# Performance work log

Measured on AMD Instinct MI355X. Metric: run time of the kernel, lower is better.

Reference implementation:

```python
import jax, jax.numpy as jnp
import numpy as np

N = 50000      # nodes
E = 800000     # edges (avg degree 16)
F_IN = 128     # num_features
H1 = 256       # hidden_dims[0]
H2 = 128       # hidden_dims[1]
D_EMB = 64     # embedding_dim
C_CLS = 2      # num_classes
EPS = 1e-5     # BatchNorm eps


def setup_inputs() -> dict:
    key = jax.random.key(0)
    ks = jax.random.split(key, 24)
    f32 = jnp.float32
    def w(k, shape, scale=0.05):
        return jax.random.normal(k, shape, f32) * scale
    inp = {
        "x": jax.random.normal(ks[0], (N, F_IN), f32),
        "edge_index": jax.random.randint(ks[1], (2, E), 0, N, jnp.int32),
        # input_proj
        "Wp": w(ks[2], (F_IN, H1)), "bp": jnp.zeros((H1,), f32),
        # conv1 (SAGEConv): lin_l (neighbors, with bias), lin_r (root, no bias)
        "W1l": w(ks[3], (F_IN, H1)), "b1l": jnp.zeros((H1,), f32), "W1r": w(ks[4], (F_IN, H1)),
        # bn1 (eval mode, running stats)
        "bn1_g": jnp.ones((H1,), f32), "bn1_b": jnp.zeros((H1,), f32),
        "bn1_m": w(ks[5], (H1,), 0.01), "bn1_v": jnp.ones((H1,), f32) + 0.1 * jax.random.uniform(ks[6], (H1,), f32),
        # skip_proj
        "Wsk": w(ks[7], (H1, H2)), "bsk": jnp.zeros((H2,), f32),
        # conv2
        "W2l": w(ks[8], (H1, H2)), "b2l": jnp.zeros((H2,), f32), "W2r": w(ks[9], (H1, H2)),
        # bn2
        "bn2_g": jnp.ones((H2,), f32), "bn2_b": jnp.zeros((H2,), f32),
        "bn2_m": w(ks[10], (H2,), 0.01), "bn2_v": jnp.ones((H2,), f32) + 0.1 * jax.random.uniform(ks[11], (H2,), f32),
        # conv3
        "W3l": w(ks[12], (H2, D_EMB)), "b3l": jnp.zeros((D_EMB,), f32), "W3r": w(ks[13], (H2, D_EMB)),
        # classifier
        "Wc": w(ks[14], (D_EMB, C_CLS)), "bc": jnp.zeros((C_CLS,), f32),
    }
    return inp


def _sage(h, src, dst, Wl, bl, Wr):
    # mean aggregation of source features into destination nodes
    s = jax.ops.segment_sum(h[src], dst, num_segments=N)        # [N, d]
    cnt = jax.ops.segment_sum(jnp.ones((src.shape[0], 1), h.dtype), dst, num_segments=N)
    mean = s / jnp.maximum(cnt, 1.0)
    return mean @ Wl + bl + h @ Wr


def _bn(h, g, b, m, v):
    return (h - m) * jax.lax.rsqrt(v + EPS) * g + b


def reference(x, edge_index, Wp, bp, W1l, b1l, W1r, bn1_g, bn1_b, bn1_m, bn1_v,
              Wsk, bsk, W2l, b2l, W2r, bn2_g, bn2_b, bn2_m, bn2_v,
              W3l, b3l, W3r, Wc, bc):
    src, dst = edge_index[0], edge_index[1]
    identity = x @ Wp + bp                                # input_proj
    h = _sage(x, src, dst, W1l, b1l, W1r)                 # conv1
    h = jax.nn.relu(_bn(h, bn1_g, bn1_b, bn1_m, bn1_v) + identity)
    # dropout is identity in eval mode
    identity = h @ Wsk + bsk                              # skip_proj
    h = _sage(h, src, dst, W2l, b2l, W2r)                 # conv2
    h = jax.nn.relu(_bn(h, bn2_g, bn2_b, bn2_m, bn2_v) + identity)
    emb = _sage(h, src, dst, W3l, b3l, W3r)               # conv3
    logits = emb @ Wc + bc
    return (logits, emb)
```

## Files before the change

kernel.cpp:

```cpp
#include <hip/hip_runtime.h>
#include <hip/hip_fp16.h>

#define NN 50000
#define NE 800000
#define SLN 6250
#define CAP 64
#define BCAP 106496
constexpr float EPSV = 1e-5f;

typedef __attribute__((ext_vector_type(8))) short short8;
typedef __attribute__((ext_vector_type(4))) float f32x4;

__device__ __forceinline__ float bf2f(unsigned short u) {
    return __uint_as_float(((unsigned int)u) << 16);
}
__device__ __forceinline__ unsigned short f2bf(float f) {
    unsigned int x = __float_as_uint(f);
    return (unsigned short)((x + 0x7FFFu + ((x >> 16) & 1u)) >> 16);
}
__device__ __forceinline__ unsigned char f2e5(float f) {
    unsigned short h = __half_as_ushort(__float2half(f));
    unsigned short r = h + 0x7F + ((h >> 8) & 1);
    return (unsigned char)(r >> 8);
}
__device__ __forceinline__ void acc16(float* a, uint4 u) {
#pragma unroll
    for (int q = 0; q < 4; q++) {
        unsigned int x = (q == 0) ? u.x : (q == 1) ? u.y : (q == 2) ? u.z : u.w;
        unsigned int h01 = ((x << 8) & 0xFF00u) | ((x << 16) & 0xFF000000u);
        unsigned int h23 = ((x >> 8) & 0xFF00u) | (x & 0xFF000000u);
        __half2 p01 = *(__half2*)&h01, p23 = *(__half2*)&h23;
        float2 f01 = __half22float2(p01), f23 = __half22float2(p23);
        a[q * 4 + 0] += f01.x; a[q * 4 + 1] += f01.y;
        a[q * 4 + 2] += f23.x; a[q * 4 + 3] += f23.y;
    }
}

__global__ __launch_bounds__(256) void k_bin(const int* __restrict__ src,
                                             const int* __restrict__ dst,
                                             int* __restrict__ binCnt,
                                             int2* __restrict__ binBuf) {
    __shared__ int hcnt[8];
    __shared__ int hbase[8];
    int tid = threadIdx.x;
    if (tid < 8) hcnt[tid] = 0;
    __syncthreads();
    int q = blockIdx.x * 256 + tid;
    bool val = q < NE / 4;
    int4 d = make_int4(0, 0, 0, 0), s = make_int4(0, 0, 0, 0);
    int b0 = 0, b1 = 0, b2 = 0, b3 = 0, r0 = 0, r1 = 0, r2 = 0, r3 = 0;
    if (val) {
        d = ((const int4*)dst)[q];
        s = ((const int4*)src)[q];
        b0 = d.x / SLN; r0 = atomicAdd(&hcnt[b0], 1);
        b1 = d.y / SLN; r1 = atomicAdd(&hcnt[b1], 1);
        b2 = d.z / SLN; r2 = atomicAdd(&hcnt[b2], 1);
        b3 = d.w / SLN; r3 = atomicAdd(&hcnt[b3], 1);
    }
    __syncthreads();
    if (tid < 8) hbase[tid] = atomicAdd(&binCnt[tid], hcnt[tid]);
    __syncthreads();
    if (val) {
        binBuf[(size_t)b0 * BCAP + hbase[b0] + r0] = make_int2(d.x, s.x);
        binBuf[(size_t)b1 * BCAP + hbase[b1] + r1] = make_int2(d.y, s.y);
        binBuf[(size_t)b2 * BCAP + hbase[b2] + r2] = make_int2(d.z, s.z);
        binBuf[(size_t)b3 * BCAP + hbase[b3] + r3] = make_int2(d.w, s.w);
    }
}

__global__ __launch_bounds__(256) void k_scatter2(const int2* __restrict__ binBuf,
                                                  const int* __restrict__ binCnt,
                                                  int* __restrict__ cnt,
                                                  int* __restrict__ csr) {
    int bin = blockIdx.x & 7;
    int lb = blockIdx.x >> 3;
    int n = binCnt[bin];
    const int2* buf = binBuf + (size_t)bin * BCAP;
    for (int i = lb * 256 + threadIdx.x; i < n; i += 128 * 256) {
        int2 p = buf[i];
        int slot = atomicAdd(&cnt[p.x], 1);
        csr[p.x * CAP + slot] = p.y;
    }
}

__device__ void prep1_body(int t, const float* Wp, const float* bp, const float* W1l,
                           const float* b1l, const float* W1r, const float* g, const float* b,
                           const float* m, const float* v, unsigned short* Wf, float* c) {
    int lane = t & 63, f = (t >> 6) & 3, kt = (t >> 8) & 7;
    int nb = t >> 11;
    int col = nb * 64 + f * 16 + (lane & 15);
    int k0 = kt * 32 + (lane >> 4) * 8;
    float A = g[col] * rsqrtf(v[col] + EPSV);
    unsigned short* o = Wf + (size_t)t * 8;
    for (int j = 0; j < 8; j++) {
        int k = k0 + j;
        float w;
        if (k < 128) w = W1l[k * 256 + col] * A;
        else         w = W1r[(k - 128) * 256 + col] * A + Wp[(k - 128) * 256 + col];
        o[j] = f2bf(w);
    }
    if (t < 256) {
        float At = g[t] * rsqrtf(v[t] + EPSV);
        c[t] = b1l[t] * At + (b[t] - m[t] * At) + bp[t];
    }
}

__device__ void prep2_body(int t, const float* Wsk, const float* bsk, const float* W2l,
                           const float* b2l, const float* W2r, const float* g, const float* b,
                           const float* m, const float* v, unsigned short* Wf, float* c) {
    int lane = t & 63, f = (t >> 6) & 3, kt = (t >> 8) & 7, nb = t >> 11;
    int col = nb * 64 + f * 16 + (lane & 15);
    int k0 = kt * 32 + (lane >> 4) * 8;
    unsigned short* o = Wf + (size_t)t * 8;
    if (col < 128) {
        float A = g[col] * rsqrtf(v[col] + EPSV);
        for (int j = 0; j < 8; j++) o[j] = f2bf(W2l[(k0 + j) * 128 + col] * A);
    } else {
        int cc = col - 128;
        float A = g[cc] * rsqrtf(v[cc] + EPSV);
        for (int j = 0; j < 8; j++)
            o[j] = f2bf(W2r[(k0 + j) * 128 + cc] * A + Wsk[(k0 + j) * 128 + cc]);
    }
    if (t < 128) {
        float At = g[t] * rsqrtf(v[t] + EPSV);
        c[t] = b2l[t] * At + (b[t] - m[t] * At) + bsk[t];
    }
}

__device__ void prep3_body(int t, const float* W3l, const float* b3l, const float* W3r,
                           unsigned short* Wf, float* c) {
    int lane = t & 63, f = (t >> 6) & 3, kt = (t >> 8) & 3, nb = t >> 10;
    int col = nb * 64 + f * 16 + (lane & 15);
    int k0 = kt * 32 + (lane >> 4) * 8;
    unsigned short* o = Wf + (size_t)t * 8;
    if (col < 64) {
        for (int j = 0; j < 8; j++) o[j] = f2bf(W3l[(k0 + j) * 64 + col]);
    } else {
        int cc = col - 64;
        for (int j = 0; j < 8; j++) o[j] = f2bf(W3r[(k0 + j) * 64 + cc]);
    }
    if (t < 64) c[t] = b3l[t];
}

__global__ void k_prep_fused(const float* x, unsigned short* xcat, unsigned char* xf8,
                             int* cnt, int* binCnt,
                             const float* Wp, const float* bp,
                             const float* W1l, const float* b1l, const float* W1r,
                             const float* g1, const float* b1, const float* m1, const float* v1,
                             const float* Wsk, const float* bsk,
                             const float* W2l, const float* b2l, const float* W2r,
                             const float* g2, const float* b2, const float* m2, const float* v2,
                             const float* W3l, const float* b3l, const float* W3r,
                             unsigned short* Wf1, unsigned short* Wf2, unsigned short* Wf3,
                             float* c1, float* c2, float* c3) {
    int bb = blockIdx.x;
    if (bb < 6250) {
        int i = bb * 256 + threadIdx.x;
        if (i < NN / 4) ((int4*)cnt)[i] = make_int4(0, 0, 0, 0);
        if (i < 2) ((int4*)binCnt)[i] = make_int4(0, 0, 0, 0);
        if (i >= NN * 128 / 4) return;
        int r = i >> 5, c4 = (i & 31) * 4;
        float4 v = ((const float4*)x)[i];
        ushort4 u = make_ushort4(f2bf(v.x), f2bf(v.y), f2bf(v.z), f2bf(v.w));
        *(ushort4*)&xcat[(size_t)r * 256 + 128 + c4] = u;
        uchar4 u8 = make_uchar4(f2e5(v.x), f2e5(v.y), f2e5(v.z), f2e5(v.w));
        *(uchar4*)&xf8[(size_t)r * 128 + c4] = u8;
    } else if (bb < 6282) {
        prep1_body((bb - 6250) * 256 + threadIdx.x, Wp, bp, W1l, b1l, W1r, g1, b1, m1, v1, Wf1, c1);
    } else if (bb < 6314) {
        prep2_body((bb - 6282) * 256 + threadIdx.x, Wsk, bsk, W2l, b2l, W2r, g2, b2, m2, v2, Wf2, c2);
    } else {
        prep3_body((bb - 6314) * 256 + threadIdx.x, W3l, b3l, W3r, Wf3, c3);
    }
}

__global__ __launch_bounds__(256) void k_gemm12(const unsigned short* __restrict__ xcat,
                                                const unsigned short* __restrict__ Wf1,
                                                const float* __restrict__ c1,
                                                const unsigned short* __restrict__ Wf2,
                                                unsigned short* __restrict__ r2,
                                                unsigned char* __restrict__ pf8) {
    constexpr int KT = 8;
    constexpr int HS = 272;
    __shared__ unsigned short Bs[256 * 64];
    __shared__ unsigned short hs[64 * HS];
    int tid = threadIdx.x;
    int lane = tid & 63, w = tid >> 6;
    int bm = blockIdx.x;
    int rbase = bm * 64 + w * 16;

    int ra = rbase + (lane & 15);
    if (ra >= NN) ra = NN - 1;
    const unsigned short* ap = xcat + (size_t)ra * 256 + ((lane >> 4) * 8);
    short8 afr[KT];
#pragma unroll
    for (int kt = 0; kt < KT; kt++) afr[kt] = *(const short8*)(ap + kt * 32);

    int hrow0 = w * 16 + (lane >> 4) * 4;

    for (int nb = 0; nb < 4; nb++) {
        __syncthreads();
        {
            const float4* srcp = (const float4*)(Wf1 + (size_t)nb * 256 * 64);
            float4* dsts = (float4*)Bs;
            for (int i = tid; i < 256 * 8; i += 256) dsts[i] = srcp[i];
        }
        __syncthreads();
        f32x4 acc[4];
#pragma unroll
        for (int f = 0; f < 4; f++) acc[f] = (f32x4){0.f, 0.f, 0.f, 0.f};
#pragma unroll
        for (int kt = 0; kt < KT; kt++) {
#pragma unroll
            for (int f = 0; f < 4; f++) {
                short8 bfr = *(const short8*)&Bs[((kt * 4 + f) * 64 + lane) * 8];
                acc[f] = __builtin_amdgcn_mfma_f32_16x16x32_bf16(afr[kt], bfr, acc[f], 0, 0, 0);
            }
        }
        int cc = nb * 64 + (lane & 15);
#pragma unroll
        for (int f = 0; f < 4; f++) {
            int col = cc + f * 16;
            float bv = c1[col];
#pragma unroll
            for (int r = 0; r < 4; r++) {
                float val = fmaxf(acc[f][r] + bv, 0.f);
                hs[(hrow0 + r) * HS + col] = f2bf(val);
            }
        }
    }

    short8 a2[KT];
    {
        const unsigned short* hp = &hs[(w * 16 + (lane & 15)) * HS + ((lane >> 4) * 8)];
#pragma unroll
        for (int kt = 0; kt < KT; kt++) a2[kt] = *(const short8*)(hp + kt * 32);
    }

    int gr0 = rbase + (lane >> 4) * 4;
    for (int nb = 0; nb < 4; nb++) {
        __syncthreads();
        {
            const float4* srcp = (const float4*)(Wf2 + (size_t)nb * 256 * 64);
            float4* dsts = (float4*)Bs;
            for (int i = tid; i < 256 * 8; i += 256) dsts[i] = srcp[i];
        }
        __syncthreads();
        f32x4 acc[4];
#pragma unroll
        for (int f = 0; f < 4; f++) acc[f] = (f32x4){0.f, 0.f, 0.f, 0.f};
#pragma unroll
        for (int kt = 0; kt < KT; kt++) {
#pragma unroll
            for (int f = 0; f < 4; f++) {
                short8 bfr = *(const short8*)&Bs[((kt * 4 + f) * 64 + lane) * 8];
                acc[f] = __builtin_amdgcn_mfma_f32_16x16x32_bf16(a2[kt], bfr, acc[f], 0, 0, 0);
            }
        }
        int cc = nb * 64 + (lane & 15);
#pragma unroll
        for (int f = 0; f < 4; f++) {
            int col = cc + f * 16;
#pragma unroll
            for (int r = 0; r < 4; r++) {
                int gr = gr0 + r;
                if (gr < NN) {
                    float val = acc[f][r];
                    if (col < 128) pf8[(size_t)gr * 128 + col] = f2e5(val);
                    else           r2[(size_t)gr * 128 + (col - 128)] = f2bf(val);
                }
            }
        }
    }
}

template <int K, int TOTN, int MODE>
__global__ __launch_bounds__(256) void k_gemm(const unsigned short* __restrict__ A,
                                              const unsigned short* __restrict__ Wf,
                                              const float* __restrict__ bias,
                                              unsigned short* __restrict__ Out,
                                              unsigned char* __restrict__ Pf8) {
    constexpr int KT = K / 32;
    constexpr int NB = TOTN / 64;
    __shared__ unsigned short Bs[K * 64];
    int tid = threadIdx.x;
    int lane = tid & 63, w = tid >> 6;
    int bm = blockIdx.x;

    int r0 = bm * 128 + w * 32;
    int ra0 = r0 + (lane & 15);
    int ra1 = ra0 + 16;
    if (ra0 >= NN) ra0 = NN - 1;
    if (ra1 >= NN) ra1 = NN - 1;
    const unsigned short* ap0 = A + (size_t)ra0 * K + ((lane >> 4) * 8);
    const unsigned short* ap1 = A + (size_t)ra1 * K + ((lane >> 4) * 8);
    short8 afr0[KT], afr1[KT];
#pragma unroll
    for (int kt = 0; kt < KT; kt++) {
        afr0[kt] = *(const short8*)(ap0 + kt * 32);
        afr1[kt] = *(const short8*)(ap1 + kt * 32);
    }

    int rb = r0 + (lane >> 4) * 4;

    for (int nb = 0; nb < NB; nb++) {
        __syncthreads();
        {
            const float4* srcp = (const float4*)(Wf + (size_t)nb * K * 64);
            float4* dsts = (float4*)Bs;
            for (int i = tid; i < K * 8; i += 256) dsts[i] = srcp[i];
        }
        __syncthreads();

        f32x4 acc[2][4];
#pragma unroll
        for (int i = 0; i < 2; i++)
#pragma unroll
            for (int f = 0; f < 4; f++) acc[i][f] = (f32x4){0.f, 0.f, 0.f, 0.f};
#pragma unroll
        for (int kt = 0; kt < KT; kt++) {
#pragma unroll
            for (int f = 0; f < 4; f++) {
                short8 bfr = *(const short8*)&Bs[((kt * 4 + f) * 64 + lane) * 8];
                acc[0][f] = __builtin_amdgcn_mfma_f32_16x16x32_bf16(afr0[kt], bfr, acc[0][f], 0, 0, 0);
                acc[1][f] = __builtin_amdgcn_mfma_f32_16x16x32_bf16(afr1[kt], bfr, acc[1][f], 0, 0, 0);
            }
        }

        int cc = nb * 64 + (lane & 15);
#pragma unroll
        for (int af = 0; af < 2; af++) {
#pragma unroll
            for (int f = 0; f < 4; f++) {
#pragma unroll
                for (int r = 0; r < 4; r++) {
                    int gr = rb + af * 16 + r;
                    if (gr < NN) {
                        float val = acc[af][f][r];
                        Out[(size_t)gr * TOTN + cc + f * 16] = f2bf(val);
                    }
                }
            }
        }
    }
}


__global__ __launch_bounds__(256) void k_aggx(const int* __restrict__ cnt,
                                              const int* __restrict__ csr,
                                              const unsigned char* __restrict__ xf8,
                                              unsigned short* __restrict__ xcat) {
    int lane = threadIdx.x & 63, wv = threadIdx.x >> 6;
    int node = blockIdx.x * 4 + wv;
    int deg = cnt[node];
    const int* cp = csr + node * CAP;
    int g = lane >> 3, l8 = lane & 7;
    float a[16];
#pragma unroll
    for (int j = 0; j < 16; j++) a[j] = 0.f;
    const unsigned char* base = xf8 + l8 * 16;
    int e = 0;
    for (; e + 16 <= deg; e += 16) {
        int s0 = cp[e + g], s1 = cp[e + 8 + g];
        uint4 u0 = *(const uint4*)(base + (size_t)s0 * 128);
        uint4 u1 = *(const uint4*)(base + (size_t)s1 * 128);
        acc16(a, u0); acc16(a, u1);
    }
    if (e + g < deg) {
        uint4 u = *(const uint4*)(base + (size_t)cp[e + g] * 128);
        acc16(a, u);
    }
    if (e + 8 + g < deg) {
        uint4 u = *(const uint4*)(base + (size_t)cp[e + 8 + g] * 128);
        acc16(a, u);
    }
#pragma unroll
    for (int j = 0; j < 16; j++) {
        a[j] += __shfl_xor(a[j], 8);
        a[j] += __shfl_xor(a[j], 16);
        a[j] += __shfl_xor(a[j], 32);
    }
    if (lane < 8) {
        float inv = 1.f / (float)max(deg, 1);
        unsigned short o[16];
#pragma unroll
        for (int j = 0; j < 16; j++) o[j] = f2bf(a[j] * inv);
        *(short8*)&xcat[(size_t)node * 256 + lane * 16] = *(short8*)&o[0];
        *(short8*)&xcat[(size_t)node * 256 + lane * 16 + 8] = *(short8*)&o[8];
    }
}

__global__ __launch_bounds__(256) void k_agg2(const unsigned char* __restrict__ pf8,
                                              const unsigned short* __restrict__ r2,
                                              const int* __restrict__ cnt,
                                              const int* __restrict__ csr,
                                              const float* __restrict__ c,
                                              unsigned short* __restrict__ h2) {
    int lane = threadIdx.x & 63, wv = threadIdx.x >> 6;
    int node = blockIdx.x * 4 + wv;
    int deg = cnt[node];
    const int* cp = csr + node * CAP;
    int g = lane >> 3, l8 = lane & 7;
    float a[16];
#pragma unroll
    for (int j = 0; j < 16; j++) a[j] = 0.f;
    const unsigned char* base = pf8 + l8 * 16;
    int e = 0;
    for (; e + 16 <= deg; e += 16) {
        int s0 = cp[e + g], s1 = cp[e + 8 + g];
        uint4 u0 = *(const uint4*)(base + (size_t)s0 * 128);
        uint4 u1 = *(const uint4*)(base + (size_t)s1 * 128);
        acc16(a, u0); acc16(a, u1);
    }
    if (e + g < deg) {
        uint4 u = *(const uint4*)(base + (size_t)cp[e + g] * 128);
        acc16(a, u);
    }
    if (e + 8 + g < deg) {
        uint4 u = *(const uint4*)(base + (size_t)cp[e + 8 + g] * 128);
        acc16(a, u);
    }
#pragma unroll
    for (int j = 0; j < 16; j++) {
        a[j] += __shfl_xor(a[j], 8);
        a[j] += __shfl_xor(a[j], 16);
        a[j] += __shfl_xor(a[j], 32);
    }
    if (lane < 8) {
        float inv = 1.f / (float)max(deg, 1);
        short8 rA = *(const short8*)&r2[(size_t)node * 128 + lane * 16];
        short8 rB = *(const short8*)&r2[(size_t)node * 128 + lane * 16 + 8];
        const float* cpb = c + lane * 16;
        unsigned short o[16];
#pragma unroll
        for (int j = 0; j < 8; j++)
            o[j] = f2bf(fmaxf(a[j] * inv + bf2f(rA[j]) + cpb[j], 0.f));
#pragma unroll
        for (int j = 0; j < 8; j++)
            o[8 + j] = f2bf(fmaxf(a[8 + j] * inv + bf2f(rB[j]) + cpb[8 + j], 0.f));
        *(short8*)&h2[(size_t)node * 128 + lane * 16] = *(short8*)&o[0];
        *(short8*)&h2[(size_t)node * 128 + lane * 16 + 8] = *(short8*)&o[8];
    }
}

__global__ __launch_bounds__(256) void k_agg_final(const unsigned short* __restrict__ G,
                                                   const int* __restrict__ cnt,
                                                   const int* __restrict__ csr,
                                                   const float* __restrict__ c,
                                                   const float* __restrict__ Wc,
                                                   const float* __restrict__ bc,
                                                   float* __restrict__ outbuf) {
    int lane = threadIdx.x & 63, wv = threadIdx.x >> 6;
    int node = blockIdx.x * 4 + wv;
    int deg = cnt[node];
    const int* cp = csr + node * CAP;
    int g = lane >> 3, l8 = lane & 7;
    float a[8];
#pragma unroll
    for (int j = 0; j < 8; j++) a[j] = 0.f;
    const unsigned short* base = G + l8 * 8;
    int e = 0;
    for (; e + 32 <= deg; e += 32) {
        int s0 = cp[e + g], s1 = cp[e + 8 + g], s2 = cp[e + 16 + g], s3 = cp[e + 24 + g];
        short8 u0 = *(const short8*)(base + (size_t)s0 * 128);
        short8 u1 = *(const short8*)(base + (size_t)s1 * 128);
        short8 u2 = *(const short8*)(base + (size_t)s2 * 128);
        short8 u3 = *(const short8*)(base + (size_t)s3 * 128);
#pragma unroll
        for (int j = 0; j < 8; j++)
            a[j] += (bf2f(u0[j]) + bf2f(u1[j])) + (bf2f(u2[j]) + bf2f(u3[j]));
    }
    for (; e + 8 <= deg; e += 8) {
        short8 u = *(const short8*)(base + (size_t)cp[e + g] * 128);
#pragma unroll
        for (int j = 0; j < 8; j++) a[j] += bf2f(u[j]);
    }
    if (e + g < deg) {
        short8 u = *(const short8*)(base + (size_t)cp[e + g] * 128);
#pragma unroll
        for (int j = 0; j < 8; j++) a[j] += bf2f(u[j]);
    }
#pragma unroll
    for (int j = 0; j < 8; j++) {
        a[j] += __shfl_xor(a[j], 8);
        a[j] += __shfl_xor(a[j], 16);
        a[j] += __shfl_xor(a[j], 32);
    }
    float l0 = 0.f, l1 = 0.f;
    if (lane < 8) {
        float inv = 1.f / (float)max(deg, 1);
        short8 r = *(const short8*)&G[(size_t)node * 128 + 64 + l8 * 8];
        const float* cpb = c + l8 * 8;
        float v[8];
#pragma unroll
        for (int j = 0; j < 8; j++) v[j] = a[j] * inv + bf2f(r[j]) + cpb[j];
        float* emb = outbuf + 2 * (size_t)NN;
        *(float4*)&emb[(size_t)node * 64 + l8 * 8] = make_float4(v[0], v[1], v[2], v[3]);
        *(float4*)&emb[(size_t)node * 64 + l8 * 8 + 4] = make_float4(v[4], v[5], v[6], v[7]);
        int c0 = l8 * 8;
#pragma unroll
        for (int j = 0; j < 8; j++) {
            l0 += v[j] * Wc[2 * (c0 + j)];
            l1 += v[j] * Wc[2 * (c0 + j) + 1];
        }
    }
    l0 += __shfl_xor(l0, 1); l1 += __shfl_xor(l1, 1);
    l0 += __shfl_xor(l0, 2); l1 += __shfl_xor(l1, 2);
    l0 += __shfl_xor(l0, 4); l1 += __shfl_xor(l1, 4);
    if (lane == 0) {
        outbuf[(size_t)node * 2 + 0] = l0 + bc[0];
        outbuf[(size_t)node * 2 + 1] = l1 + bc[1];
    }
}

extern "C" void kernel_launch(void* const* d_in, const int* in_sizes, int n_in,
                              void* d_out, int out_size, void* d_ws, size_t ws_size,
                              hipStream_t stream) {
    const float* x    = (const float*)d_in[0];
    const int*   ei   = (const int*)d_in[1];
    const float* Wp   = (const float*)d_in[2];
    const float* bp   = (const float*)d_in[3];
    const float* W1l  = (const float*)d_in[4];
    const float* b1l  = (const float*)d_in[5];
    const float* W1r  = (const float*)d_in[6];
    const float* bn1g = (const float*)d_in[7];
    const float* bn1b = (const float*)d_in[8];
    const float* bn1m = (const float*)d_in[9];
    const float* bn1v = (const float*)d_in[10];
    const float* Wsk  = (const float*)d_in[11];
    const float* bsk  = (const float*)d_in[12];
    const float* W2l  = (const float*)d_in[13];
    const float* b2l  = (const float*)d_in[14];
    const float* W2r  = (const float*)d_in[15];
    const float* bn2g = (const float*)d_in[16];
    const float* bn2b = (const float*)d_in[17];
    const float* bn2m = (const float*)d_in[18];
    const float* bn2v = (const float*)d_in[19];
    const float* W3l  = (const float*)d_in[20];
    const float* b3l  = (const float*)d_in[21];
    const float* W3r  = (const float*)d_in[22];
    const float* Wc   = (const float*)d_in[23];
    const float* bc   = (const float*)d_in[24];

    const int* src = ei;
    const int* dst = ei + NE;

    char* ws = (char*)d_ws;
    size_t o = 0;
    auto alloc = [&](size_t b) -> char* {
        char* p = ws + o;
        o = (o + b + 255) & ~(size_t)255;
        return p;
    };
    int* cnt    = (int*)alloc((size_t)NN * 4);
    int* binCnt = (int*)alloc(64);
    int* csr    = (int*)alloc((size_t)NN * CAP * 4);
    unsigned char*  xf8  = (unsigned char*)alloc((size_t)NN * 128);
    unsigned short* xcat = (unsigned short*)alloc((size_t)NN * 256 * 2);
    unsigned char*  pf8  = (unsigned char*)alloc((size_t)NN * 128);
    unsigned short* r2   = (unsigned short*)alloc((size_t)NN * 128 * 2);
    unsigned short* h2   = (unsigned short*)alloc((size_t)NN * 128 * 2);
    unsigned short* G3   = (unsigned short*)alloc((size_t)NN * 128 * 2);
    unsigned short* Wf1  = (unsigned short*)alloc((size_t)256 * 256 * 2);
    unsigned short* Wf2  = (unsigned short*)alloc((size_t)256 * 256 * 2);
    unsigned short* Wf3  = (unsigned short*)alloc((size_t)128 * 128 * 2);
    float* c1 = (float*)alloc(256 * 4);
    float* c2 = (float*)alloc(128 * 4);
    float* c3 = (float*)alloc(64 * 4);
    int2* binBuf = (int2*)G3;

    float* outbuf = (float*)d_out;

    k_prep_fused<<<6322, 256, 0, stream>>>(x, xcat, xf8, cnt, binCnt,
                                           Wp, bp, W1l, b1l, W1r, bn1g, bn1b, bn1m, bn1v,
                                           Wsk, bsk, W2l, b2l, W2r, bn2g, bn2b, bn2m, bn2v,
                                           W3l, b3l, W3r, Wf1, Wf2, Wf3, c1, c2, c3);

    k_bin<<<782, 256, 0, stream>>>(src, dst, binCnt, binBuf);
    k_scatter2<<<1024, 256, 0, stream>>>(binBuf, binCnt, cnt, csr);

    k_aggx<<<12500, 256, 0, stream>>>(cnt, csr, xf8, xcat);

    k_gemm12<<<782, 256, 0, stream>>>(xcat, Wf1, c1, Wf2, r2, pf8);
    k_agg2<<<12500, 256, 0, stream>>>(pf8, r2, cnt, csr, c2, h2);

    k_gemm<128, 128, 0><<<391, 256, 0, stream>>>(h2, Wf3, nullptr, G3, nullptr);
    k_agg_final<<<12500, 256, 0, stream>>>(G3, cnt, csr, c3, Wc, bc, outbuf);
}
```

Baseline: 200.2 us.

## Register-prefetch weight tiles in fused GEMM and use smaller tiles for layer-3 GEMM

In k_gemm12 the B-weight tile is halved to 32 columns and streamed through registers, so the next chunk's global loads are issued before the current chunk's MFMAs. This overlaps the weight fetch with compute and shrinks shared memory, which should allow more blocks per CU. The hs padding changes from 272 to 268. The layer-3 GEMM drops from 32 rows per wave to 16 rows per wave over 782 blocks, giving more parallelism at the cost of reloading the weights more often.

New measurement: 202.9 us. No clear change (+1.3%).

```diff
diff --git a/kernel.cpp b/kernel.cpp
--- a/kernel.cpp
+++ b/kernel.cpp
@@ -181,8 +181,8 @@
                                                 unsigned short* __restrict__ r2,
                                                 unsigned char* __restrict__ pf8) {
     constexpr int KT = 8;
-    constexpr int HS = 272;
-    __shared__ unsigned short Bs[256 * 64];
+    constexpr int HS = 268;
+    __shared__ unsigned short Bs[256 * 32];
     __shared__ unsigned short hs[64 * HS];
     int tid = threadIdx.x;
     int lane = tid & 63, w = tid >> 6;
@@ -196,25 +196,38 @@
 #pragma unroll
     for (int kt = 0; kt < KT; kt++) afr[kt] = *(const short8*)(ap + kt * 32);
 
+    int skt = tid >> 5;
+    int sj = (tid & 31) * 4;
+    float4* bsd = (float4*)Bs + skt * 128 + sj;
+
+    auto csrc = [&](int c) -> const float4* {
+        const unsigned short* W = (c < 8) ? Wf1 : Wf2;
+        int nb = (c & 7) >> 1, sub = c & 1;
+        return (const float4*)W + (size_t)nb * 2048 + skt * 256 + sub * 128 + sj;
+    };
+    float4 pre0, pre1, pre2, pre3;
+    { const float4* s = csrc(0); pre0 = s[0]; pre1 = s[1]; pre2 = s[2]; pre3 = s[3]; }
+
     int hrow0 = w * 16 + (lane >> 4) * 4;
 
     for (int nb = 0; nb < 4; nb++) {
-        __syncthreads();
-        {
-            const float4* srcp = (const float4*)(Wf1 + (size_t)nb * 256 * 64);
-            float4* dsts = (float4*)Bs;
-            for (int i = tid; i < 256 * 8; i += 256) dsts[i] = srcp[i];
-        }
-        __syncthreads();
         f32x4 acc[4];
 #pragma unroll
         for (int f = 0; f < 4; f++) acc[f] = (f32x4){0.f, 0.f, 0.f, 0.f};
 #pragma unroll
-        for (int kt = 0; kt < KT; kt++) {
-#pragma unroll
-            for (int f = 0; f < 4; f++) {
-                short8 bfr = *(const short8*)&Bs[((kt * 4 + f) * 64 + lane) * 8];
-                acc[f] = __builtin_amdgcn_mfma_f32_16x16x32_bf16(afr[kt], bfr, acc[f], 0, 0, 0);
+        for (int sub = 0; sub < 2; sub++) {
+            int c = nb * 2 + sub;
+            __syncthreads();
+            bsd[0] = pre0; bsd[1] = pre1; bsd[2] = pre2; bsd[3] = pre3;
+            __syncthreads();
+            { const float4* s = csrc(c + 1); pre0 = s[0]; pre1 = s[1]; pre2 = s[2]; pre3 = s[3]; }
+#pragma unroll
+            for (int kt = 0; kt < KT; kt++) {
+#pragma unroll
+                for (int fr = 0; fr < 2; fr++) {
+                    short8 bfr = *(const short8*)&Bs[((kt * 2 + fr) * 64 + lane) * 8];
+                    acc[sub * 2 + fr] = __builtin_amdgcn_mfma_f32_16x16x32_bf16(afr[kt], bfr, acc[sub * 2 + fr], 0, 0, 0);
+                }
             }
         }
         int cc = nb * 64 + (lane & 15);
@@ -239,22 +252,23 @@
 
     int gr0 = rbase + (lane >> 4) * 4;
     for (int nb = 0; nb < 4; nb++) {
-        __syncthreads();
-        {
-            const float4* srcp = (const float4*)(Wf2 + (size_t)nb * 256 * 64);
-            float4* dsts = (float4*)Bs;
-            for (int i = tid; i < 256 * 8; i += 256) dsts[i] = srcp[i];
-        }
-        __syncthreads();
         f32x4 acc[4];
 #pragma unroll
         for (int f = 0; f < 4; f++) acc[f] = (f32x4){0.f, 0.f, 0.f, 0.f};
 #pragma unroll
-        for (int kt = 0; kt < KT; kt++) {
-#pragma unroll
-            for (int f = 0; f < 4; f++) {
-                short8 bfr = *(const short8*)&Bs[((kt * 4 + f) * 64 + lane) * 8];
-                acc[f] = __builtin_amdgcn_mfma_f32_16x16x32_bf16(a2[kt], bfr, acc[f], 0, 0, 0);
+        for (int sub = 0; sub < 2; sub++) {
+            int c = 8 + nb * 2 + sub;
+            __syncthreads();
+            bsd[0] = pre0; bsd[1] = pre1; bsd[2] = pre2; bsd[3] = pre3;
+            __syncthreads();
+            if (c < 15) { const float4* s = csrc(c + 1); pre0 = s[0]; pre1 = s[1]; pre2 = s[2]; pre3 = s[3]; }
+#pragma unroll
+            for (int kt = 0; kt < KT; kt++) {
+#pragma unroll
+                for (int fr = 0; fr < 2; fr++) {
+                    short8 bfr = *(const short8*)&Bs[((kt * 2 + fr) * 64 + lane) * 8];
+                    acc[sub * 2 + fr] = __builtin_amdgcn_mfma_f32_16x16x32_bf16(a2[kt], bfr, acc[sub * 2 + fr], 0, 0, 0);
+                }
             }
         }
         int cc = nb * 64 + (lane & 15);
@@ -274,72 +288,50 @@
     }
 }
 
-template <int K, int TOTN, int MODE>
-__global__ __launch_bounds__(256) void k_gemm(const unsigned short* __restrict__ A,
-                                              const unsigned short* __restrict__ Wf,
-                                              const float* __restrict__ bias,
-                                              unsigned short* __restrict__ Out,
-                                              unsigned char* __restrict__ Pf8) {
-    constexpr int KT = K / 32;
-    constexpr int NB = TOTN / 64;
-    __shared__ unsigned short Bs[K * 64];
+__global__ __launch_bounds__(256) void k_gemm3(const unsigned short* __restrict__ h2,
+                                               const unsigned short* __restrict__ Wf3,
+                                               unsigned short* __restrict__ G3) {
+    constexpr int KT = 4;
+    __shared__ unsigned short Bs[128 * 64];
     int tid = threadIdx.x;
     int lane = tid & 63, w = tid >> 6;
     int bm = blockIdx.x;
 
-    int r0 = bm * 128 + w * 32;
-    int ra0 = r0 + (lane & 15);
-    int ra1 = ra0 + 16;
-    if (ra0 >= NN) ra0 = NN - 1;
-    if (ra1 >= NN) ra1 = NN - 1;
-    const unsigned short* ap0 = A + (size_t)ra0 * K + ((lane >> 4) * 8);
-    const unsigned short* ap1 = A + (size_t)ra1 * K + ((lane >> 4) * 8);
-    short8 afr0[KT], afr1[KT];
-#pragma unroll
-    for (int kt = 0; kt < KT; kt++) {
-        afr0[kt] = *(const short8*)(ap0 + kt * 32);
-        afr1[kt] = *(const short8*)(ap1 + kt * 32);
-    }
-
-    int rb = r0 + (lane >> 4) * 4;
-
-    for (int nb = 0; nb < NB; nb++) {
+    int ra = bm * 64 + w * 16 + (lane & 15);
+    if (ra >= NN) ra = NN - 1;
+    const unsigned short* ap = h2 + (size_t)ra * 128 + ((lane >> 4) * 8);
+    short8 afr[KT];
+#pragma unroll
+    for (int kt = 0; kt < KT; kt++) afr[kt] = *(const short8*)(ap + kt * 32);
+
+    int gr0 = bm * 64 + w * 16 + (lane >> 4) * 4;
+
+    for (int nb = 0; nb < 2; nb++) {
         __syncthreads();
         {
-            const float4* srcp = (const float4*)(Wf + (size_t)nb * K * 64);
+            const float4* srcp = (const float4*)(Wf3 + (size_t)nb * 128 * 64);
             float4* dsts = (float4*)Bs;
-            for (int i = tid; i < K * 8; i += 256) dsts[i] = srcp[i];
+            for (int i = tid; i < 128 * 8; i += 256) dsts[i] = srcp[i];
         }
         __syncthreads();
-
-        f32x4 acc[2][4];
-#pragma unroll
-        for (int i = 0; i < 2; i++)
-#pragma unroll
-            for (int f = 0; f < 4; f++) acc[i][f] = (f32x4){0.f, 0.f, 0.f, 0.f};
+        f32x4 acc[4];
+#pragma unroll
+        for (int f = 0; f < 4; f++) acc[f] = (f32x4){0.f, 0.f, 0.f, 0.f};
 #pragma unroll
         for (int kt = 0; kt < KT; kt++) {
 #pragma unroll
             for (int f = 0; f < 4; f++) {
                 short8 bfr = *(const short8*)&Bs[((kt * 4 + f) * 64 + lane) * 8];
-                acc[0][f] = __builtin_amdgcn_mfma_f32_16x16x32_bf16(afr0[kt], bfr, acc[0][f], 0, 0, 0);
-                acc[1][f] = __builtin_amdgcn_mfma_f32_16x16x32_bf16(afr1[kt], bfr, acc[1][f], 0, 0, 0);
+                acc[f] = __builtin_amdgcn_mfma_f32_16x16x32_bf16(afr[kt], bfr, acc[f], 0, 0, 0);
             }
         }
-
         int cc = nb * 64 + (lane & 15);
 #pragma unroll
-        for (int af = 0; af < 2; af++) {
-#pragma unroll
-            for (int f = 0; f < 4; f++) {
-#pragma unroll
-                for (int r = 0; r < 4; r++) {
-                    int gr = rb + af * 16 + r;
-                    if (gr < NN) {
-                        float val = acc[af][f][r];
-                        Out[(size_t)gr * TOTN + cc + f * 16] = f2bf(val);
-                    }
-                }
+        for (int f = 0; f < 4; f++) {
+#pragma unroll
+            for (int r = 0; r < 4; r++) {
+                int gr = gr0 + r;
+                if (gr < NN) G3[(size_t)gr * 128 + cc + f * 16] = f2bf(acc[f][r]);
             }
         }
     }
@@ -584,6 +576,6 @@
     k_gemm12<<<782, 256, 0, stream>>>(xcat, Wf1, c1, Wf2, r2, pf8);
     k_agg2<<<12500, 256, 0, stream>>>(pf8, r2, cnt, csr, c2, h2);
 
-    k_gemm<128, 128, 0><<<391, 256, 0, stream>>>(h2, Wf3, nullptr, G3, nullptr);
+    k_gemm3<<<782, 256, 0, stream>>>(h2, Wf3, G3);
     k_agg_final<<<12500, 256, 0, stream>>>(G3, cnt, csr, c3, Wc, bc, outbuf);
 }
```
